# Optimization experiments

Hardware: AMD Instinct MI355X
Metric: run time of the kernel (lower is better)

## Reference

```python
import jax, jax.numpy as jnp
import numpy as np

N_IMGS = 2000
N_PTS = 500000
M_OBS = 8000000


def setup_inputs() -> dict:
    key = jax.random.key(0)
    k1, k2, k3, k4, k5, k6, k7 = jax.random.split(key, 7)
    # pose: [tx,ty,tz, qx,qy,qz,qw, f, k1, k2]
    t = 0.1 * jax.random.normal(k1, (N_IMGS, 3), dtype=jnp.float32)
    # near-identity quaternion (small perturbation), normalized
    qv = 0.05 * jax.random.normal(k2, (N_IMGS, 3), dtype=jnp.float32)
    q = jnp.concatenate([qv, jnp.ones((N_IMGS, 1), jnp.float32)], axis=-1)
    q = q / jnp.linalg.norm(q, axis=-1, keepdims=True)
    f = 500.0 + 500.0 * jax.random.uniform(k3, (N_IMGS, 1), dtype=jnp.float32)
    kd = 1e-3 * jax.random.normal(k4, (N_IMGS, 2), dtype=jnp.float32)
    pose = jnp.concatenate([t, q, f, kd], axis=-1)  # [N_IMGS, 10]
    # 3D points with z safely away from 0 (in front of cameras)
    xy = jax.random.normal(k5, (N_PTS, 2), dtype=jnp.float32)
    z = 2.0 + 8.0 * jax.random.uniform(k5, (N_PTS, 1), dtype=jnp.float32)
    points_3d = jnp.concatenate([xy, z], axis=-1)  # [N_PTS, 3]
    points_2d = 100.0 * jax.random.normal(k6, (M_OBS, 2), dtype=jnp.float32)
    camera_indices = jax.random.randint(k7, (M_OBS,), 0, N_IMGS)
    point_indices = jax.random.randint(jax.random.fold_in(k7, 1), (M_OBS,), 0, N_PTS)
    return {
        "points_2d": points_2d,
        "camera_indices": camera_indices,
        "point_indices": point_indices,
        "pose": pose,
        "points_3d": points_3d,
    }


def reference(points_2d, camera_indices, point_indices, pose, points_3d):
    cam = pose[camera_indices]        # [M,10] gather per observation
    pts = points_3d[point_indices]    # [M,3]
    t = cam[:, :3]
    q = cam[:, 3:7]                   # [qx,qy,qz,qw]
    q = q / jnp.linalg.norm(q, axis=-1, keepdims=True)
    qv, qw = q[:, :3], q[:, 3:4]
    # SE3 action: R(q) * p + t, via v + 2*qv x (qv x v + w*v)
    uv = jnp.cross(qv, pts)
    p_cam = pts + 2.0 * jnp.cross(qv, uv + qw * pts) + t  # [M,3]
    # COLMAP convention: u = X/Z, v = Y/Z (no negation)
    uvp = p_cam[:, :2] / p_cam[:, 2:3]                    # [M,2]
    f = cam[:, 7:8]
    rk1 = cam[:, 8:9]
    rk2 = cam[:, 9:10]
    n = jnp.sum(uvp * uvp, axis=-1, keepdims=True)        # r^2
    d = 1.0 + rk1 * n + rk2 * n * n                       # radial distortion
    return uvp * d * f - points_2d
```

## Files before the change

kernel.cpp:

```cpp
#include <hip/hip_runtime.h>


typedef float  f2_t __attribute__((ext_vector_type(2)));
typedef _Float16 h4_t __attribute__((ext_vector_type(4)));

#define NCAM_MAX 2032
#define UNROLL 4

__global__ __launch_bounds__(256) void prep_pts_h(
    const float* __restrict__ pts3, h4_t* __restrict__ ptsh, int n)
{
    int i = blockIdx.x * blockDim.x + threadIdx.x;
    if (i >= n) return;
    const float* p = pts3 + (long)i * 3;
    h4_t h;
    h.x = (_Float16)p[0];
    h.y = (_Float16)p[1];
    h.z = (_Float16)p[2];
    h.w = (_Float16)0.0f;
    ptsh[i] = h;
}

__device__ __forceinline__ void compute_one(
    float px, float py, float pz,
    float qx, float qy, float qz,
    float tx, float ty, float tz,
    float fl, unsigned kk,
    f2_t o, f2_t* r)
{
    float qw = sqrtf(fmaxf(0.0f, 1.0f - (qx*qx + qy*qy + qz*qz)));
    float ux = qy*pz - qz*py;
    float uy = qz*px - qx*pz;
    float uz = qx*py - qy*px;
    float wx = ux + qw*px;
    float wy = uy + qw*py;
    float wz = uz + qw*pz;
    float cx = qy*wz - qz*wy;
    float cy = qz*wx - qx*wz;
    float cz = qx*wy - qy*wx;
    float Px = px + 2.0f*cx + tx;
    float Py = py + 2.0f*cy + ty;
    float Pz = pz + 2.0f*cz + tz;
    float invz = 1.0f / Pz;
    float u = Px * invz;
    float v = Py * invz;
    float k1 = __uint_as_float(kk << 16);
    float k2 = __uint_as_float(kk & 0xffff0000u);
    float n = u*u + v*v;
    float d = 1.0f + k1*n + k2*n*n;
    float s = d * fl;
    r->x = u*s - o.x;
    r->y = v*s - o.y;
}

__global__ __launch_bounds__(1024) void reproj5_kernel(
    const float* __restrict__ p2d,
    const int* __restrict__ cidx,
    const int* __restrict__ pidx,
    const float* __restrict__ pose,
    const h4_t* __restrict__ ptsh,
    float* __restrict__ out,
    int M, int n_imgs)
{
    __shared__ float s_tx[NCAM_MAX], s_ty[NCAM_MAX], s_tz[NCAM_MAX];
    __shared__ float s_qx[NCAM_MAX], s_qy[NCAM_MAX], s_qz[NCAM_MAX];
    __shared__ float s_fl[NCAM_MAX];
    __shared__ unsigned s_kk[NCAM_MAX];

    for (int r = threadIdx.x; r < n_imgs; r += blockDim.x) {
        const float* c = pose + (long)r * 10;
        float tx = c[0], ty = c[1], tz = c[2];
        float qx = c[3], qy = c[4], qz = c[5], qw = c[6];
        float fl = c[7], k1 = c[8], k2 = c[9];
        float inv = rsqrtf(qx*qx + qy*qy + qz*qz + qw*qw);
        if (qw < 0.0f) inv = -inv;
        qx *= inv; qy *= inv; qz *= inv;
        s_tx[r] = tx; s_ty[r] = ty; s_tz[r] = tz;
        s_qx[r] = qx; s_qy[r] = qy; s_qz[r] = qz;
        s_fl[r] = fl;
        unsigned b1 = (__float_as_uint(k1) + 0x8000u) >> 16;
        unsigned b2 = (__float_as_uint(k2) + 0x8000u) >> 16;
        s_kk[r] = (b1 & 0xffffu) | ((b2 & 0xffffu) << 16);
    }
    __syncthreads();

    int tid = blockIdx.x * blockDim.x + threadIdx.x;
    int stride = gridDim.x * blockDim.x;
    long step = (long)stride * UNROLL;

    for (long base = tid; base < M; base += step) {
        if (base + (long)(UNROLL - 1) * stride < M) {
            int ci[UNROLL], pi[UNROLL];
            #pragma unroll
            for (int k = 0; k < UNROLL; k++) {
                long i = base + (long)k * stride;
                ci[k] = __builtin_nontemporal_load(cidx + i);
                pi[k] = __builtin_nontemporal_load(pidx + i);
            }
            h4_t p[UNROLL];
            f2_t o[UNROLL];
            #pragma unroll
            for (int k = 0; k < UNROLL; k++) {
                p[k] = ptsh[pi[k]];
                o[k] = __builtin_nontemporal_load((const f2_t*)p2d + (base + (long)k * stride));
            }
            #pragma unroll
            for (int k = 0; k < UNROLL; k++) {
                int c = ci[k];
                f2_t r;
                compute_one((float)p[k].x, (float)p[k].y, (float)p[k].z,
                            s_qx[c], s_qy[c], s_qz[c],
                            s_tx[c], s_ty[c], s_tz[c],
                            s_fl[c], s_kk[c], o[k], &r);
                __builtin_nontemporal_store(r, (f2_t*)out + (base + (long)k * stride));
            }
        } else {
            for (int k = 0; k < UNROLL; k++) {
                long i = base + (long)k * stride;
                if (i >= M) break;
                int c = __builtin_nontemporal_load(cidx + i);
                int pi1 = __builtin_nontemporal_load(pidx + i);
                h4_t p = ptsh[pi1];
                f2_t o = __builtin_nontemporal_load((const f2_t*)p2d + i);
                f2_t r;
                compute_one((float)p.x, (float)p.y, (float)p.z,
                            s_qx[c], s_qy[c], s_qz[c],
                            s_tx[c], s_ty[c], s_tz[c],
                            s_fl[c], s_kk[c], o, &r);
                __builtin_nontemporal_store(r, (f2_t*)out + i);
            }
        }
    }
}

__global__ __launch_bounds__(256) void reproj_direct_kernel(
    const float2* __restrict__ p2d,
    const int* __restrict__ cidx,
    const int* __restrict__ pidx,
    const float* __restrict__ pose,
    const float* __restrict__ pts3,
    float2* __restrict__ out,
    int M)
{
    int i = blockIdx.x * blockDim.x + threadIdx.x;
    if (i >= M) return;
    int ci = cidx[i];
    int pi = pidx[i];
    const float* cam = pose + (long)ci * 10;
    float tx = cam[0], ty = cam[1], tz = cam[2];
    float qx = cam[3], qy = cam[4], qz = cam[5], qw = cam[6];
    float f  = cam[7], k1 = cam[8], k2 = cam[9];
    float inv = rsqrtf(qx*qx + qy*qy + qz*qz + qw*qw);
    qx *= inv; qy *= inv; qz *= inv; qw *= inv;
    const float* pp = pts3 + (long)pi * 3;
    float px = pp[0], py = pp[1], pz = pp[2];
    float ux = qy*pz - qz*py;
    float uy = qz*px - qx*pz;
    float uz = qx*py - qy*px;
    float wx = ux + qw*px;
    float wy = uy + qw*py;
    float wz = uz + qw*pz;
    float cx = qy*wz - qz*wy;
    float cy = qz*wx - qx*wz;
    float cz = qx*wy - qy*wx;
    float Px = px + 2.0f*cx + tx;
    float Py = py + 2.0f*cy + ty;
    float Pz = pz + 2.0f*cz + tz;
    float invz = 1.0f / Pz;
    float u = Px * invz;
    float v = Py * invz;
    float n = u*u + v*v;
    float d = 1.0f + k1*n + k2*n*n;
    float s = d * f;
    float2 o = p2d[i];
    out[i] = make_float2(u*s - o.x, v*s - o.y);
}

extern "C" void kernel_launch(void* const* d_in, const int* in_sizes, int n_in,
                              void* d_out, int out_size, void* d_ws, size_t ws_size,
                              hipStream_t stream) {
    const float* p2d  = (const float*)d_in[0];
    const int*   cidx = (const int*)d_in[1];
    const int*   pidx = (const int*)d_in[2];
    const float* pose = (const float*)d_in[3];
    const float* pts3 = (const float*)d_in[4];

    int M      = in_sizes[1];
    int n_imgs = in_sizes[3] / 10;
    int n_pts  = in_sizes[4] / 3;

    size_t need = (size_t)n_pts * 8;

    if (ws_size >= need && n_imgs <= NCAM_MAX) {
        h4_t* ptsh = (h4_t*)d_ws;
        prep_pts_h<<<(n_pts + 255) / 256, 256, 0, stream>>>(pts3, ptsh, n_pts);
        int block = 1024;
        int grid  = 512;
        reproj5_kernel<<<grid, block, 0, stream>>>(
            p2d, cidx, pidx, pose, ptsh, (float*)d_out, M, n_imgs);
    } else {
        reproj_direct_kernel<<<(M + 255) / 256, 256, 0, stream>>>(
            (const float2*)p2d, cidx, pidx, pose, pts3, (float2*)d_out, M);
    }
}
```

Measured before the change: 96.91 us.

## Process eight contiguous observations per thread with vectorized 128-bit loads and stores

Replaces the persistent grid-stride loop with a one-shot grid in which each thread handles eight consecutive observations. Index, observation and output arrays move through 128-bit vector loads and stores, and each thread issues eight point gathers at once to raise memory-level parallelism. The cost is roughly twice as many blocks, each of which reloads the full camera table into LDS, adding prologue traffic and sync overhead.

```diff
diff --git a/kernel.cpp b/kernel.cpp
--- a/kernel.cpp
+++ b/kernel.cpp
@@ -1,11 +1,13 @@
 #include <hip/hip_runtime.h>
 
 
-typedef float  f2_t __attribute__((ext_vector_type(2)));
+typedef float    f2_t __attribute__((ext_vector_type(2)));
+typedef float    f4_t __attribute__((ext_vector_type(4)));
+typedef int      i4_t __attribute__((ext_vector_type(4)));
 typedef _Float16 h4_t __attribute__((ext_vector_type(4)));
 
 #define NCAM_MAX 2032
-#define UNROLL 4
+#define UNROLL 8
 
 __global__ __launch_bounds__(256) void prep_pts_h(
     const float* __restrict__ pts3, h4_t* __restrict__ ptsh, int n)
@@ -26,7 +28,7 @@
     float qx, float qy, float qz,
     float tx, float ty, float tz,
     float fl, unsigned kk,
-    f2_t o, f2_t* r)
+    float ox, float oy, float* rx, float* ry)
 {
     float qw = sqrtf(fmaxf(0.0f, 1.0f - (qx*qx + qy*qy + qz*qz)));
     float ux = qy*pz - qz*py;
@@ -49,11 +51,11 @@
     float n = u*u + v*v;
     float d = 1.0f + k1*n + k2*n*n;
     float s = d * fl;
-    r->x = u*s - o.x;
-    r->y = v*s - o.y;
-}
-
-__global__ __launch_bounds__(1024) void reproj5_kernel(
+    *rx = u*s - ox;
+    *ry = v*s - oy;
+}
+
+__global__ __launch_bounds__(1024) void reproj8_kernel(
     const float* __restrict__ p2d,
     const int* __restrict__ cidx,
     const int* __restrict__ pidx,
@@ -84,51 +86,58 @@
     }
     __syncthreads();
 
-    int tid = blockIdx.x * blockDim.x + threadIdx.x;
-    int stride = gridDim.x * blockDim.x;
-    long step = (long)stride * UNROLL;
-
-    for (long base = tid; base < M; base += step) {
-        if (base + (long)(UNROLL - 1) * stride < M) {
-            int ci[UNROLL], pi[UNROLL];
-            #pragma unroll
-            for (int k = 0; k < UNROLL; k++) {
-                long i = base + (long)k * stride;
-                ci[k] = __builtin_nontemporal_load(cidx + i);
-                pi[k] = __builtin_nontemporal_load(pidx + i);
-            }
-            h4_t p[UNROLL];
-            f2_t o[UNROLL];
-            #pragma unroll
-            for (int k = 0; k < UNROLL; k++) {
-                p[k] = ptsh[pi[k]];
-                o[k] = __builtin_nontemporal_load((const f2_t*)p2d + (base + (long)k * stride));
-            }
-            #pragma unroll
-            for (int k = 0; k < UNROLL; k++) {
-                int c = ci[k];
-                f2_t r;
-                compute_one((float)p[k].x, (float)p[k].y, (float)p[k].z,
-                            s_qx[c], s_qy[c], s_qz[c],
-                            s_tx[c], s_ty[c], s_tz[c],
-                            s_fl[c], s_kk[c], o[k], &r);
-                __builtin_nontemporal_store(r, (f2_t*)out + (base + (long)k * stride));
-            }
-        } else {
-            for (int k = 0; k < UNROLL; k++) {
-                long i = base + (long)k * stride;
-                if (i >= M) break;
-                int c = __builtin_nontemporal_load(cidx + i);
-                int pi1 = __builtin_nontemporal_load(pidx + i);
-                h4_t p = ptsh[pi1];
-                f2_t o = __builtin_nontemporal_load((const f2_t*)p2d + i);
-                f2_t r;
-                compute_one((float)p.x, (float)p.y, (float)p.z,
-                            s_qx[c], s_qy[c], s_qz[c],
-                            s_tx[c], s_ty[c], s_tz[c],
-                            s_fl[c], s_kk[c], o, &r);
-                __builtin_nontemporal_store(r, (f2_t*)out + i);
-            }
+    long T = (long)blockIdx.x * blockDim.x + threadIdx.x;
+    long base = T * UNROLL;
+
+    if (base + UNROLL <= M) {
+        i4_t c01 = __builtin_nontemporal_load((const i4_t*)(cidx + base));
+        i4_t c23 = __builtin_nontemporal_load((const i4_t*)(cidx + base) + 1);
+        i4_t q01 = __builtin_nontemporal_load((const i4_t*)(pidx + base));
+        i4_t q23 = __builtin_nontemporal_load((const i4_t*)(pidx + base) + 1);
+        int ci[UNROLL] = {c01.x, c01.y, c01.z, c01.w, c23.x, c23.y, c23.z, c23.w};
+        int pi[UNROLL] = {q01.x, q01.y, q01.z, q01.w, q23.x, q23.y, q23.z, q23.w};
+
+        h4_t p[UNROLL];
+        #pragma unroll
+        for (int k = 0; k < UNROLL; k++) p[k] = ptsh[pi[k]];
+
+        f4_t o[UNROLL/2];
+        #pragma unroll
+        for (int k = 0; k < UNROLL/2; k++)
+            o[k] = __builtin_nontemporal_load((const f4_t*)(p2d + 2*base) + k);
+
+        f4_t r[UNROLL/2];
+        #pragma unroll
+        for (int k = 0; k < UNROLL; k++) {
+            int c = ci[k];
+            float ox = (k & 1) ? o[k>>1].z : o[k>>1].x;
+            float oy = (k & 1) ? o[k>>1].w : o[k>>1].y;
+            float rx, ry;
+            compute_one((float)p[k].x, (float)p[k].y, (float)p[k].z,
+                        s_qx[c], s_qy[c], s_qz[c],
+                        s_tx[c], s_ty[c], s_tz[c],
+                        s_fl[c], s_kk[c], ox, oy, &rx, &ry);
+            if (k & 1) { r[k>>1].z = rx; r[k>>1].w = ry; }
+            else       { r[k>>1].x = rx; r[k>>1].y = ry; }
+        }
+        #pragma unroll
+        for (int k = 0; k < UNROLL/2; k++)
+            __builtin_nontemporal_store(r[k], (f4_t*)(out + 2*base) + k);
+    } else {
+        for (int k = 0; k < UNROLL; k++) {
+            long i = base + k;
+            if (i >= M) break;
+            int c = cidx[i];
+            int pi1 = pidx[i];
+            h4_t p = ptsh[pi1];
+            f2_t o = __builtin_nontemporal_load((const f2_t*)p2d + i);
+            float rx, ry;
+            compute_one((float)p.x, (float)p.y, (float)p.z,
+                        s_qx[c], s_qy[c], s_qz[c],
+                        s_tx[c], s_ty[c], s_tz[c],
+                        s_fl[c], s_kk[c], o.x, o.y, &rx, &ry);
+            f2_t r; r.x = rx; r.y = ry;
+            __builtin_nontemporal_store(r, (f2_t*)out + i);
         }
     }
 }
@@ -195,8 +204,9 @@
         h4_t* ptsh = (h4_t*)d_ws;
         prep_pts_h<<<(n_pts + 255) / 256, 256, 0, stream>>>(pts3, ptsh, n_pts);
         int block = 1024;
-        int grid  = 512;
-        reproj5_kernel<<<grid, block, 0, stream>>>(
+        long threads_needed = ((long)M + UNROLL - 1) / UNROLL;
+        int grid = (int)((threads_needed + block - 1) / block);
+        reproj8_kernel<<<grid, block, 0, stream>>>(
             p2d, cidx, pidx, pose, ptsh, (float*)d_out, M, n_imgs);
     } else {
         reproj_direct_kernel<<<(M + 255) / 256, 256, 0, stream>>>(
```

New measurement: 116.7 us. 1.2x slower.
